# Kernel optimization log

Measured on AMD Instinct MI355X. Metric: run time of the kernel, lower is better.

## Reference

```python
import jax, jax.numpy as jnp
import numpy as np

N_PTS = 131072
K_POSE = 4
J = 24
P_NUM = 64
R_COMP = 32
POSE_DIM = 32
GRID = (512, 512, 128)
MAT_MODE = ((0, 1), (0, 2), (1, 2))


def sample_line(line, xs):
    # line: [k, R, G], xs: [N] in [-1, 1].
    # Equivalent to F.grid_sample on a [k,R,G,1] map with grid x-coord fixed to 0
    # (W==1 so the x dim is degenerate) -> 1D linear interpolation along G.
    G = line.shape[-1]
    pos = (xs + 1.0) * 0.5 * (G - 1)
    i0 = jnp.clip(jnp.floor(pos), 0, G - 1).astype(jnp.int32)
    i1 = jnp.clip(i0 + 1, 0, G - 1)
    w = pos - i0.astype(xs.dtype)
    v0 = jnp.take(line, i0, axis=-1)  # [k,R,N]
    v1 = jnp.take(line, i1, axis=-1)
    return v0 * (1.0 - w) + v1 * w


def blend(w, A):
    # w: [1,N,J], A: [1,J,4,4] -> per-point blended LBS transform [1,N,4,4]
    return jnp.einsum('bnj,bjuv->bnuv', w, A)


def lbs_points(pts, T, inverse):
    Rm = T[..., :3, :3]
    t = T[..., :3, 3]
    if inverse:
        return jnp.einsum('bnij,bnj->bni', jnp.linalg.inv(Rm), pts - t)
    return jnp.einsum('bnij,bnj->bni', Rm, pts) + t


def lbs_dirs(d, T, inverse):
    Rm = T[..., :3, :3]
    if inverse:
        return jnp.einsum('bnij,bnj->bni', jnp.linalg.inv(Rm), d)
    return jnp.einsum('bnij,bnj->bni', Rm, d)


def setup_inputs() -> dict:
    key = jax.random.key(0)
    ks = jax.random.split(key, 12)
    pose_pts = 0.3 * jax.random.normal(ks[0], (1, N_PTS, 3), jnp.float32)
    pose_dirs = jax.random.normal(ks[1], (1, N_PTS, 3), jnp.float32)
    sw = jax.random.uniform(ks[2], (1, N_PTS, J), dtype=jnp.float32)
    skinning_weight = sw / jnp.sum(sw, axis=-1, keepdims=True)
    eye = jnp.eye(4, dtype=jnp.float32)
    A = eye + 0.2 * jax.random.normal(ks[3], (1, J, 4, 4), jnp.float32)
    big_A = eye + 0.2 * jax.random.normal(ks[4], (1, J, 4, 4), jnp.float32)
    tbounds = jnp.array([[-1.5, -1.5, -1.5], [1.5, 1.5, 1.5]], jnp.float32)
    coord_line0 = 0.1 * jax.random.normal(ks[5], (P_NUM, R_COMP, GRID[0], 1), jnp.float32)
    coord_line1 = 0.1 * jax.random.normal(ks[6], (P_NUM, R_COMP, GRID[1], 1), jnp.float32)
    coord_line2 = 0.1 * jax.random.normal(ks[7], (P_NUM, R_COMP, GRID[2], 1), jnp.float32)
    feat_line0 = 0.1 * jax.random.normal(ks[8], (P_NUM, R_COMP, POSE_DIM, 1), jnp.float32)
    feat_line1 = 0.1 * jax.random.normal(ks[9], (P_NUM, R_COMP, POSE_DIM, 1), jnp.float32)
    feat_line2 = 0.1 * jax.random.normal(ks[10], (P_NUM, R_COMP, POSE_DIM, 1), jnp.float32)
    tw = jax.random.uniform(ks[11], (K_POSE,), dtype=jnp.float32) + 0.1
    topk_weight = tw / jnp.sum(tw)  # L1-normalized top-k pose weights
    topk_id = jax.random.randint(jax.random.fold_in(key, 7), (K_POSE,), 0, P_NUM, dtype=jnp.int32)
    return dict(pose_pts=pose_pts, pose_dirs=pose_dirs, skinning_weight=skinning_weight,
                A=A, big_A=big_A, tbounds=tbounds,
                coord_line0=coord_line0, coord_line1=coord_line1, coord_line2=coord_line2,
                feat_line0=feat_line0, feat_line1=feat_line1, feat_line2=feat_line2,
                topk_weight=topk_weight, topk_id=topk_id)


def reference(pose_pts, pose_dirs, skinning_weight, A, big_A, tbounds,
              coord_line0, coord_line1, coord_line2,
              feat_line0, feat_line1, feat_line2,
              topk_weight, topk_id):
    # --- backward_deform: observed pose -> t-pose (inv A) -> big/canonical pose (big_A) ---
    T_A = blend(skinning_weight, A)
    T_big = blend(skinning_weight, big_A)
    tpose = lbs_points(pose_pts, T_A, inverse=True)
    cnl_pts = lbs_points(tpose, T_big, inverse=False)   # [1,N,3]
    tdirs = lbs_dirs(pose_dirs, T_A, inverse=True)
    cnl_dirs = lbs_dirs(tdirs, T_big, inverse=False)    # [1,N,3]
    # --- get_pose_feat: normalize_pts detaches pts, then TensoRF-style line sampling ---
    npts = jax.lax.stop_gradient(cnl_pts)
    npts = (npts - tbounds[0]) / (tbounds[1] - tbounds[0]) * 2.0 - 1.0  # [1,N,3]
    coord_lines = (coord_line0, coord_line1, coord_line2)
    feat_lines = (feat_line0, feat_line1, feat_line2)
    coords, feats = [], []
    for i in range(3):
        line = coord_lines[i][topk_id][..., 0]           # [k,R,G_i]
        coords.append(sample_line(line, npts[0, :, i]))  # [k,R,N]
        feats.append(feat_lines[i][topk_id][..., 0])     # [k,R,C]
    planes = []
    for p, (i0, i1) in enumerate(MAT_MODE):
        t = coords[i0] * coords[i1]                      # [k,R,N] outer-product term
        planes.append(jnp.einsum('krn,krc->knc', t, feats[p]))  # reduce over R
    pose_feats = jnp.concatenate(planes, axis=-1)        # [k,N,3C]
    pose_feat = jnp.sum(topk_weight[:, None, None] * pose_feats, axis=0, keepdims=True)
    return jnp.concatenate([cnl_pts, cnl_dirs, pose_feat], axis=-1)  # [1,N,102]
```

## Files before the change

### kernel.cpp

```cpp
#include <hip/hip_runtime.h>

#define NPTS 131072
#define G0 512
#define G1 512
#define G2 128

#define SKIN_BLOCKS  512
#define TRANS_BLOCKS 576
#define FEAT_BLOCKS  48

typedef float v4f __attribute__((ext_vector_type(4)));
typedef __attribute__((ext_vector_type(8))) short short8;

__device__ float  g_linesT[4*(G0+G1+G2)*32];
__device__ unsigned short g_featB[3*4*2*64*8];
__device__ float4 g_pos[NPTS];

__device__ __forceinline__ unsigned short bf16rne(float x){
  unsigned int u = __float_as_uint(x);
  u += 0x7fffu + ((u >> 16) & 1u);
  return (unsigned short)(u >> 16);
}

__global__ __launch_bounds__(256) void prep_skin(
    const float* __restrict__ pts, const float* __restrict__ dirs,
    const float* __restrict__ sw,  const float* __restrict__ Am,
    const float* __restrict__ Bm,  const float* __restrict__ tb,
    const float* __restrict__ c0,  const float* __restrict__ c1,
    const float* __restrict__ c2,  const float* __restrict__ f0,
    const float* __restrict__ f1,  const float* __restrict__ f2,
    const float* __restrict__ tw,  const int* __restrict__ topk_id,
    float* __restrict__ out)
{
  const int bid = blockIdx.x;
  const int tid = threadIdx.x;

  if (bid >= SKIN_BLOCKS) {
    int pb = bid - SKIN_BLOCKS;
    if (pb < TRANS_BLOCKS) {
      int e = pb*256 + tid;
      const float* src; int logG, outoff;
      if (e < 65536)       { src = c0; logG = 9; outoff = 0; }
      else if (e < 131072) { e -= 65536;  src = c1; logG = 9; outoff = 4*G0*32; }
      else                 { e -= 131072; src = c2; logG = 7; outoff = 4*(G0+G1)*32; }
      const int G = 1 << logG;
      int g  = e & (G-1);
      int t  = e >> logG;
      int r  = t & 31;
      int kk = t >> 5;
      int id = topk_id[kk];
      float v = src[(id*32 + r)*G + g];
      g_linesT[outoff + (kk*G + g)*32 + r] = v;
    } else {
      int e = (pb - TRANS_BLOCKS)*256 + tid;
      if (e < 3*4*2*64*8) {
        int j    =  e        & 7;
        int lane = (e >> 3)  & 63;
        int tcol = (e >> 9)  & 1;
        int s    = (e >> 10) & 3;
        int p    =  e >> 12;
        int r = ((lane >> 4) << 3) + j;
        int cc = tcol*16 + (lane & 15);
        const float* f = (p == 0) ? f0 : ((p == 1) ? f1 : f2);
        float v = tw[s] * f[(topk_id[s]*32 + r)*32 + cc];
        g_featB[e] = bf16rne(v);
      }
    }
    return;
  }

  __shared__ float sA[384];
  __shared__ float sB[384];
  for (int i = tid; i < 384; i += 256){ sA[i] = Am[i]; sB[i] = Bm[i]; }
  __syncthreads();

  const int n = bid*256 + tid;
  float swv[24];
  {
    const float4* swp = reinterpret_cast<const float4*>(sw + n*24);
    #pragma unroll
    for (int i = 0; i < 6; i++){
      float4 v = swp[i];
      swv[4*i] = v.x; swv[4*i+1] = v.y; swv[4*i+2] = v.z; swv[4*i+3] = v.w;
    }
  }
  float RA[9] = {0,0,0,0,0,0,0,0,0}, tA[3] = {0,0,0};
  float RB[9] = {0,0,0,0,0,0,0,0,0}, tB[3] = {0,0,0};
  #pragma unroll
  for (int j = 0; j < 24; j++){
    float w = swv[j];
    const float* a = sA + j*16;
    const float* b = sB + j*16;
    RA[0] = fmaf(w, a[0], RA[0]); RA[1] = fmaf(w, a[1], RA[1]); RA[2] = fmaf(w, a[2], RA[2]); tA[0] = fmaf(w, a[3],  tA[0]);
    RA[3] = fmaf(w, a[4], RA[3]); RA[4] = fmaf(w, a[5], RA[4]); RA[5] = fmaf(w, a[6], RA[5]); tA[1] = fmaf(w, a[7],  tA[1]);
    RA[6] = fmaf(w, a[8], RA[6]); RA[7] = fmaf(w, a[9], RA[7]); RA[8] = fmaf(w, a[10],RA[8]); tA[2] = fmaf(w, a[11], tA[2]);
    RB[0] = fmaf(w, b[0], RB[0]); RB[1] = fmaf(w, b[1], RB[1]); RB[2] = fmaf(w, b[2], RB[2]); tB[0] = fmaf(w, b[3],  tB[0]);
    RB[3] = fmaf(w, b[4], RB[3]); RB[4] = fmaf(w, b[5], RB[4]); RB[5] = fmaf(w, b[6], RB[5]); tB[1] = fmaf(w, b[7],  tB[1]);
    RB[6] = fmaf(w, b[8], RB[6]); RB[7] = fmaf(w, b[9], RB[7]); RB[8] = fmaf(w, b[10],RB[8]); tB[2] = fmaf(w, b[11], tB[2]);
  }
  float c00 = RA[4]*RA[8] - RA[5]*RA[7];
  float c01 = RA[5]*RA[6] - RA[3]*RA[8];
  float c02 = RA[3]*RA[7] - RA[4]*RA[6];
  float det = RA[0]*c00 + RA[1]*c01 + RA[2]*c02;
  float idet = 1.0f/det;
  float i00 = c00*idet;
  float i01 = (RA[2]*RA[7] - RA[1]*RA[8])*idet;
  float i02 = (RA[1]*RA[5] - RA[2]*RA[4])*idet;
  float i10 = c01*idet;
  float i11 = (RA[0]*RA[8] - RA[2]*RA[6])*idet;
  float i12 = (RA[2]*RA[3] - RA[0]*RA[5])*idet;
  float i20 = c02*idet;
  float i21 = (RA[1]*RA[6] - RA[0]*RA[7])*idet;
  float i22 = (RA[0]*RA[4] - RA[1]*RA[3])*idet;

  float px = pts[n*3+0], py = pts[n*3+1], pz = pts[n*3+2];
  float dx = dirs[n*3+0], dy = dirs[n*3+1], dz = dirs[n*3+2];
  float qx = px - tA[0], qy = py - tA[1], qz = pz - tA[2];
  float tpx = i00*qx + i01*qy + i02*qz;
  float tpy = i10*qx + i11*qy + i12*qz;
  float tpz = i20*qx + i21*qy + i22*qz;
  float cx = RB[0]*tpx + RB[1]*tpy + RB[2]*tpz + tB[0];
  float cy = RB[3]*tpx + RB[4]*tpy + RB[5]*tpz + tB[1];
  float cz = RB[6]*tpx + RB[7]*tpy + RB[8]*tpz + tB[2];
  float tdx = i00*dx + i01*dy + i02*dz;
  float tdy = i10*dx + i11*dy + i12*dz;
  float tdz = i20*dx + i21*dy + i22*dz;
  float cdx = RB[0]*tdx + RB[1]*tdy + RB[2]*tdz;
  float cdy = RB[3]*tdx + RB[4]*tdy + RB[5]*tdz;
  float cdz = RB[6]*tdx + RB[7]*tdy + RB[8]*tdz;

  {
    float* o = out + (size_t)n*102;
    o[0] = cx; o[1] = cy; o[2] = cz; o[3] = cdx; o[4] = cdy; o[5] = cdz;
  }
  {
    float lo0 = tb[0], lo1 = tb[1], lo2 = tb[2];
    float hi0 = tb[3], hi1 = tb[4], hi2 = tb[5];
    float x0 = (cx - lo0)/(hi0 - lo0)*2.0f - 1.0f;
    float x1 = (cy - lo1)/(hi1 - lo1)*2.0f - 1.0f;
    float x2 = (cz - lo2)/(hi2 - lo2)*2.0f - 1.0f;
    float4 p;
    p.x = (x0 + 1.0f)*0.5f*(float)(G0-1);
    p.y = (x1 + 1.0f)*0.5f*(float)(G1-1);
    p.z = (x2 + 1.0f)*0.5f*(float)(G2-1);
    p.w = 0.0f;
    g_pos[n] = p;
  }
}

__global__ __launch_bounds__(256, 4) void einsum_mfma(float* __restrict__ out)
{
  const int tid  = threadIdx.x;
  const int lane = tid & 63;
  const int wv   = tid >> 6;
  const int m    = lane & 15;
  const int q    = lane >> 4;
  const int tile = blockIdx.x*4 + wv;
  const int pl   = tile*16 + m;

  float4 pos = g_pos[pl];
  float f0i = fminf(fmaxf(floorf(pos.x), 0.0f), (float)(G0-1));
  int a0i0 = (int)f0i; int a0i1 = min(a0i0+1, G0-1); float w0 = pos.x - f0i;
  float f1i = fminf(fmaxf(floorf(pos.y), 0.0f), (float)(G1-1));
  int a1i0 = (int)f1i; int a1i1 = min(a1i0+1, G1-1); float w1 = pos.y - f1i;
  float f2i = fminf(fmaxf(floorf(pos.z), 0.0f), (float)(G2-1));
  int a2i0 = (int)f2i; int a2i1 = min(a2i0+1, G2-1); float w2 = pos.z - f2i;

  const float* lt0 = g_linesT;
  const float* lt1 = g_linesT + 4*G0*32;
  const float* lt2 = g_linesT + 4*(G0+G1)*32;
  const short8* fb = reinterpret_cast<const short8*>(g_featB);

  v4f acc00 = {0,0,0,0}, acc01 = {0,0,0,0};
  v4f acc10 = {0,0,0,0}, acc11 = {0,0,0,0};
  v4f acc20 = {0,0,0,0}, acc21 = {0,0,0,0};

  #pragma unroll
  for (int s = 0; s < 4; s++){
    float c0[8], c1[8], c2[8];
    {
      const float* p0 = lt0 + (s*G0 + a0i0)*32 + q*8;
      const float* p1 = lt0 + (s*G0 + a0i1)*32 + q*8;
      float4 v0a = *(const float4*)p0, v0b = *(const float4*)(p0+4);
      float4 v1a = *(const float4*)p1, v1b = *(const float4*)(p1+4);
      c0[0] = fmaf(w0, v1a.x - v0a.x, v0a.x);
      c0[1] = fmaf(w0, v1a.y - v0a.y, v0a.y);
      c0[2] = fmaf(w0, v1a.z - v0a.z, v0a.z);
      c0[3] = fmaf(w0, v1a.w - v0a.w, v0a.w);
      c0[4] = fmaf(w0, v1b.x - v0b.x, v0b.x);
      c0[5] = fmaf(w0, v1b.y - v0b.y, v0b.y);
      c0[6] = fmaf(w0, v1b.z - v0b.z, v0b.z);
      c0[7] = fmaf(w0, v1b.w - v0b.w, v0b.w);
    }
    {
      const float* p0 = lt1 + (s*G1 + a1i0)*32 + q*8;
      const float* p1 = lt1 + (s*G1 + a1i1)*32 + q*8;
      float4 v0a = *(const float4*)p0, v0b = *(const float4*)(p0+4);
      float4 v1a = *(const float4*)p1, v1b = *(const float4*)(p1+4);
      c1[0] = fmaf(w1, v1a.x - v0a.x, v0a.x);
      c1[1] = fmaf(w1, v1a.y - v0a.y, v0a.y);
      c1[2] = fmaf(w1, v1a.z - v0a.z, v0a.z);
      c1[3] = fmaf(w1, v1a.w - v0a.w, v0a.w);
      c1[4] = fmaf(w1, v1b.x - v0b.x, v0b.x);
      c1[5] = fmaf(w1, v1b.y - v0b.y, v0b.y);
      c1[6] = fmaf(w1, v1b.z - v0b.z, v0b.z);
      c1[7] = fmaf(w1, v1b.w - v0b.w, v0b.w);
    }
    {
      const float* p0 = lt2 + (s*G2 + a2i0)*32 + q*8;
      const float* p1 = lt2 + (s*G2 + a2i1)*32 + q*8;
      float4 v0a = *(const float4*)p0, v0b = *(const float4*)(p0+4);
      float4 v1a = *(const float4*)p1, v1b = *(const float4*)(p1+4);
      c2[0] = fmaf(w2, v1a.x - v0a.x, v0a.x);
      c2[1] = fmaf(w2, v1a.y - v0a.y, v0a.y);
      c2[2] = fmaf(w2, v1a.z - v0a.z, v0a.z);
      c2[3] = fmaf(w2, v1a.w - v0a.w, v0a.w);
      c2[4] = fmaf(w2, v1b.x - v0b.x, v0b.x);
      c2[5] = fmaf(w2, v1b.y - v0b.y, v0b.y);
      c2[6] = fmaf(w2, v1b.z - v0b.z, v0b.z);
      c2[7] = fmaf(w2, v1b.w - v0b.w, v0b.w);
    }
    short8 A0, A1, A2;
    #pragma unroll
    for (int j = 0; j < 8; j++){
      A0[j] = (short)bf16rne(c0[j]*c1[j]);
      A1[j] = (short)bf16rne(c0[j]*c2[j]);
      A2[j] = (short)bf16rne(c1[j]*c2[j]);
    }
    short8 B00 = fb[(0*8 + s*2 + 0)*64 + lane];
    short8 B01 = fb[(0*8 + s*2 + 1)*64 + lane];
    short8 B10 = fb[(1*8 + s*2 + 0)*64 + lane];
    short8 B11 = fb[(1*8 + s*2 + 1)*64 + lane];
    short8 B20 = fb[(2*8 + s*2 + 0)*64 + lane];
    short8 B21 = fb[(2*8 + s*2 + 1)*64 + lane];
    acc00 = __builtin_amdgcn_mfma_f32_16x16x32_bf16(A0, B00, acc00, 0, 0, 0);
    acc01 = __builtin_amdgcn_mfma_f32_16x16x32_bf16(A0, B01, acc01, 0, 0, 0);
    acc10 = __builtin_amdgcn_mfma_f32_16x16x32_bf16(A1, B10, acc10, 0, 0, 0);
    acc11 = __builtin_amdgcn_mfma_f32_16x16x32_bf16(A1, B11, acc11, 0, 0, 0);
    acc20 = __builtin_amdgcn_mfma_f32_16x16x32_bf16(A2, B20, acc20, 0, 0, 0);
    acc21 = __builtin_amdgcn_mfma_f32_16x16x32_bf16(A2, B21, acc21, 0, 0, 0);
  }

  const int rowBase = tile*16 + q*4;
  #pragma unroll
  for (int v = 0; v < 4; v++){
    float* o = out + (size_t)(rowBase + v)*102 + 6 + m;
    o[0]  = acc00[v];
    o[16] = acc01[v];
    o[32] = acc10[v];
    o[48] = acc11[v];
    o[64] = acc20[v];
    o[80] = acc21[v];
  }
}

extern "C" void kernel_launch(void* const* d_in, const int* in_sizes, int n_in,
                              void* d_out, int out_size, void* d_ws, size_t ws_size,
                              hipStream_t stream) {
  const float* pose_pts  = (const float*)d_in[0];
  const float* pose_dirs = (const float*)d_in[1];
  const float* sw        = (const float*)d_in[2];
  const float* Am        = (const float*)d_in[3];
  const float* Bm        = (const float*)d_in[4];
  const float* tb        = (const float*)d_in[5];
  const float* cl0       = (const float*)d_in[6];
  const float* cl1       = (const float*)d_in[7];
  const float* cl2       = (const float*)d_in[8];
  const float* fl0       = (const float*)d_in[9];
  const float* fl1       = (const float*)d_in[10];
  const float* fl2       = (const float*)d_in[11];
  const float* tw        = (const float*)d_in[12];
  const int*   tkid      = (const int*)d_in[13];
  float* out = (float*)d_out;

  hipLaunchKernelGGL(prep_skin, dim3(SKIN_BLOCKS + TRANS_BLOCKS + FEAT_BLOCKS), dim3(256), 0, stream,
                     pose_pts, pose_dirs, sw, Am, Bm, tb,
                     cl0, cl1, cl2, fl0, fl1, fl2, tw, tkid, out);
  hipLaunchKernelGGL(einsum_mfma, dim3(NPTS/(4*16)), dim3(256), 0, stream, out);
}
```

Baseline: 163.0 us.

## Store transposed line tables in bf16 and pack MFMA operands with perm

Result: faster. 137.0 us (-15.9%).

```diff
diff --git a/kernel.cpp b/kernel.cpp
--- a/kernel.cpp
+++ b/kernel.cpp
@@ -9,10 +9,14 @@
 #define TRANS_BLOCKS 576
 #define FEAT_BLOCKS  48
 
+#define OFF1 (4*G0*32)
+#define OFF2 (4*(G0+G1)*32)
+#define LTOT (4*(G0+G1+G2)*32)
+
 typedef float v4f __attribute__((ext_vector_type(4)));
 typedef __attribute__((ext_vector_type(8))) short short8;
 
-__device__ float  g_linesT[4*(G0+G1+G2)*32];
+__device__ unsigned short g_lines16[LTOT + 32];
 __device__ unsigned short g_featB[3*4*2*64*8];
 __device__ float4 g_pos[NPTS];
 
@@ -20,6 +24,28 @@
   unsigned int u = __float_as_uint(x);
   u += 0x7fffu + ((u >> 16) & 1u);
   return (unsigned short)(u >> 16);
+}
+
+__device__ __forceinline__ void cvt8(uint4 r, float* f){
+  f[0] = __uint_as_float(r.x << 16); f[1] = __uint_as_float(r.x & 0xffff0000u);
+  f[2] = __uint_as_float(r.y << 16); f[3] = __uint_as_float(r.y & 0xffff0000u);
+  f[4] = __uint_as_float(r.z << 16); f[5] = __uint_as_float(r.z & 0xffff0000u);
+  f[6] = __uint_as_float(r.w << 16); f[7] = __uint_as_float(r.w & 0xffff0000u);
+}
+
+__device__ __forceinline__ void lerp_rows(const unsigned short* p, float w, float* c){
+  uint4 r0 = *(const uint4*)p;
+  uint4 r1 = *(const uint4*)(p + 32);
+  float a[8], b[8];
+  cvt8(r0, a); cvt8(r1, b);
+  #pragma unroll
+  for (int j = 0; j < 8; j++) c[j] = fmaf(w, b[j] - a[j], a[j]);
+}
+
+__device__ __forceinline__ unsigned int pack2(float lo, float hi){
+  unsigned int ul = __float_as_uint(lo) + 0x8000u;
+  unsigned int uh = __float_as_uint(hi) + 0x8000u;
+  return __builtin_amdgcn_perm(uh, ul, 0x07060302u);
 }
 
 __global__ __launch_bounds__(256) void prep_skin(
@@ -41,8 +67,8 @@
       int e = pb*256 + tid;
       const float* src; int logG, outoff;
       if (e < 65536)       { src = c0; logG = 9; outoff = 0; }
-      else if (e < 131072) { e -= 65536;  src = c1; logG = 9; outoff = 4*G0*32; }
-      else                 { e -= 131072; src = c2; logG = 7; outoff = 4*(G0+G1)*32; }
+      else if (e < 131072) { e -= 65536;  src = c1; logG = 9; outoff = OFF1; }
+      else                 { e -= 131072; src = c2; logG = 7; outoff = OFF2; }
       const int G = 1 << logG;
       int g  = e & (G-1);
       int t  = e >> logG;
@@ -50,7 +76,7 @@
       int kk = t >> 5;
       int id = topk_id[kk];
       float v = src[(id*32 + r)*G + g];
-      g_linesT[outoff + (kk*G + g)*32 + r] = v;
+      g_lines16[outoff + (kk*G + g)*32 + r] = bf16rne(v);
     } else {
       int e = (pb - TRANS_BLOCKS)*256 + tid;
       if (e < 3*4*2*64*8) {
@@ -69,6 +95,8 @@
     return;
   }
 
+  if (bid == 0 && tid < 32) g_lines16[LTOT + tid] = 0;
+
   __shared__ float sA[384];
   __shared__ float sB[384];
   for (int i = tid; i < 384; i += 256){ sA[i] = Am[i]; sB[i] = Bm[i]; }
@@ -148,7 +176,7 @@
   }
 }
 
-__global__ __launch_bounds__(256, 4) void einsum_mfma(float* __restrict__ out)
+__global__ __launch_bounds__(256) void einsum_mfma(float* __restrict__ out)
 {
   const int tid  = threadIdx.x;
   const int lane = tid & 63;
@@ -159,16 +187,16 @@
   const int pl   = tile*16 + m;
 
   float4 pos = g_pos[pl];
-  float f0i = fminf(fmaxf(floorf(pos.x), 0.0f), (float)(G0-1));
-  int a0i0 = (int)f0i; int a0i1 = min(a0i0+1, G0-1); float w0 = pos.x - f0i;
-  float f1i = fminf(fmaxf(floorf(pos.y), 0.0f), (float)(G1-1));
-  int a1i0 = (int)f1i; int a1i1 = min(a1i0+1, G1-1); float w1 = pos.y - f1i;
-  float f2i = fminf(fmaxf(floorf(pos.z), 0.0f), (float)(G2-1));
-  int a2i0 = (int)f2i; int a2i1 = min(a2i0+1, G2-1); float w2 = pos.z - f2i;
-
-  const float* lt0 = g_linesT;
-  const float* lt1 = g_linesT + 4*G0*32;
-  const float* lt2 = g_linesT + 4*(G0+G1)*32;
+  float pc0 = fminf(fmaxf(pos.x, 0.0f), (float)(G0-1));
+  float pc1 = fminf(fmaxf(pos.y, 0.0f), (float)(G1-1));
+  float pc2 = fminf(fmaxf(pos.z, 0.0f), (float)(G2-1));
+  float fl0 = floorf(pc0), fl1 = floorf(pc1), fl2 = floorf(pc2);
+  int a0 = (int)fl0, a1 = (int)fl1, a2 = (int)fl2;
+  float w0 = pc0 - fl0, w1 = pc1 - fl1, w2 = pc2 - fl2;
+
+  const unsigned short* lt0 = g_lines16;
+  const unsigned short* lt1 = g_lines16 + OFF1;
+  const unsigned short* lt2 = g_lines16 + OFF2;
   const short8* fb = reinterpret_cast<const short8*>(g_featB);
 
   v4f acc00 = {0,0,0,0}, acc01 = {0,0,0,0};
@@ -178,55 +206,27 @@
   #pragma unroll
   for (int s = 0; s < 4; s++){
     float c0[8], c1[8], c2[8];
-    {
-      const float* p0 = lt0 + (s*G0 + a0i0)*32 + q*8;
-      const float* p1 = lt0 + (s*G0 + a0i1)*32 + q*8;
-      float4 v0a = *(const float4*)p0, v0b = *(const float4*)(p0+4);
-      float4 v1a = *(const float4*)p1, v1b = *(const float4*)(p1+4);
-      c0[0] = fmaf(w0, v1a.x - v0a.x, v0a.x);
-      c0[1] = fmaf(w0, v1a.y - v0a.y, v0a.y);
-      c0[2] = fmaf(w0, v1a.z - v0a.z, v0a.z);
-      c0[3] = fmaf(w0, v1a.w - v0a.w, v0a.w);
-      c0[4] = fmaf(w0, v1b.x - v0b.x, v0b.x);
-      c0[5] = fmaf(w0, v1b.y - v0b.y, v0b.y);
-      c0[6] = fmaf(w0, v1b.z - v0b.z, v0b.z);
-      c0[7] = fmaf(w0, v1b.w - v0b.w, v0b.w);
-    }
-    {
-      const float* p0 = lt1 + (s*G1 + a1i0)*32 + q*8;
-      const float* p1 = lt1 + (s*G1 + a1i1)*32 + q*8;
-      float4 v0a = *(const float4*)p0, v0b = *(const float4*)(p0+4);
-      float4 v1a = *(const float4*)p1, v1b = *(const float4*)(p1+4);
-      c1[0] = fmaf(w1, v1a.x - v0a.x, v0a.x);
-      c1[1] = fmaf(w1, v1a.y - v0a.y, v0a.y);
-      c1[2] = fmaf(w1, v1a.z - v0a.z, v0a.z);
-      c1[3] = fmaf(w1, v1a.w - v0a.w, v0a.w);
-      c1[4] = fmaf(w1, v1b.x - v0b.x, v0b.x);
-      c1[5] = fmaf(w1, v1b.y - v0b.y, v0b.y);
-      c1[6] = fmaf(w1, v1b.z - v0b.z, v0b.z);
-      c1[7] = fmaf(w1, v1b.w - v0b.w, v0b.w);
-    }
-    {
-      const float* p0 = lt2 + (s*G2 + a2i0)*32 + q*8;
-      const float* p1 = lt2 + (s*G2 + a2i1)*32 + q*8;
-      float4 v0a = *(const float4*)p0, v0b = *(const float4*)(p0+4);
-      float4 v1a = *(const float4*)p1, v1b = *(const float4*)(p1+4);
-      c2[0] = fmaf(w2, v1a.x - v0a.x, v0a.x);
-      c2[1] = fmaf(w2, v1a.y - v0a.y, v0a.y);
-      c2[2] = fmaf(w2, v1a.z - v0a.z, v0a.z);
-      c2[3] = fmaf(w2, v1a.w - v0a.w, v0a.w);
-      c2[4] = fmaf(w2, v1b.x - v0b.x, v0b.x);
-      c2[5] = fmaf(w2, v1b.y - v0b.y, v0b.y);
-      c2[6] = fmaf(w2, v1b.z - v0b.z, v0b.z);
-      c2[7] = fmaf(w2, v1b.w - v0b.w, v0b.w);
-    }
-    short8 A0, A1, A2;
-    #pragma unroll
-    for (int j = 0; j < 8; j++){
-      A0[j] = (short)bf16rne(c0[j]*c1[j]);
-      A1[j] = (short)bf16rne(c0[j]*c2[j]);
-      A2[j] = (short)bf16rne(c1[j]*c2[j]);
-    }
+    lerp_rows(lt0 + (s*G0 + a0)*32 + q*8, w0, c0);
+    lerp_rows(lt1 + (s*G1 + a1)*32 + q*8, w1, c1);
+    lerp_rows(lt2 + (s*G2 + a2)*32 + q*8, w2, c2);
+
+    uint4 A0u, A1u, A2u;
+    A0u.x = pack2(c0[0]*c1[0], c0[1]*c1[1]);
+    A0u.y = pack2(c0[2]*c1[2], c0[3]*c1[3]);
+    A0u.z = pack2(c0[4]*c1[4], c0[5]*c1[5]);
+    A0u.w = pack2(c0[6]*c1[6], c0[7]*c1[7]);
+    A1u.x = pack2(c0[0]*c2[0], c0[1]*c2[1]);
+    A1u.y = pack2(c0[2]*c2[2], c0[3]*c2[3]);
+    A1u.z = pack2(c0[4]*c2[4], c0[5]*c2[5]);
+    A1u.w = pack2(c0[6]*c2[6], c0[7]*c2[7]);
+    A2u.x = pack2(c1[0]*c2[0], c1[1]*c2[1]);
+    A2u.y = pack2(c1[2]*c2[2], c1[3]*c2[3]);
+    A2u.z = pack2(c1[4]*c2[4], c1[5]*c2[5]);
+    A2u.w = pack2(c1[6]*c2[6], c1[7]*c2[7]);
+    short8 A0 = __builtin_bit_cast(short8, A0u);
+    short8 A1 = __builtin_bit_cast(short8, A1u);
+    short8 A2 = __builtin_bit_cast(short8, A2u);
+
     short8 B00 = fb[(0*8 + s*2 + 0)*64 + lane];
     short8 B01 = fb[(0*8 + s*2 + 1)*64 + lane];
     short8 B10 = fb[(1*8 + s*2 + 0)*64 + lane];
```
